# Optimization experiments

Hardware: AMD Instinct MI355X
Metric: run time of the kernel (lower is better)

The kernel has to match this reference:

```python
import jax, jax.numpy as jnp
import numpy as np

N_HEADS = 16
NEG_BIG = float(-2**32 + 1)  # value the original writes into masked positions


def setup_inputs() -> dict:
    key = jax.random.key(0)
    ks = jax.random.split(key, 5)
    B, T, D = 64, 256, 1024
    s = 1.0 / np.sqrt(D)
    return {
        "x": jax.random.normal(ks[0], (B, T, D), jnp.float32),
        "pos_emb": jax.random.normal(ks[1], (T, D), jnp.float32),
        "Wq": jax.random.normal(ks[2], (D, D), jnp.float32) * s,
        "Wk": jax.random.normal(ks[3], (D, D), jnp.float32) * s,
        "Wv": jax.random.normal(ks[4], (D, D), jnp.float32) * s,
    }


def reference(x, pos_emb, Wq, Wk, Wv):
    B, T, D = x.shape
    H = N_HEADS
    dh = D // H
    # add position embeddings (same arange positions for every batch row)
    temporal = x + pos_emb[None, :T, :]            # [B, T, D]
    q = temporal @ Wq                              # [B, T, D]
    k = temporal @ Wk
    v = temporal @ Wv
    # chunk along feature dim into H heads, concatenate along batch dim -> [H*B, T, dh]
    def split_heads(t):
        return jnp.concatenate(jnp.split(t, H, axis=2), axis=0)
    q_, k_, v_ = split_heads(q), split_heads(k), split_heads(v)
    scores = jnp.einsum('btd,bsd->bts', q_, k_) / jnp.sqrt(jnp.asarray(T, x.dtype))  # [H*B, T, T]
    # original masks the LOWER triangle (tril > 0 -> padding), faithful to source
    tril = jnp.tril(jnp.ones((T, T), x.dtype))
    scores = jnp.where(tril > 0, jnp.asarray(NEG_BIG, x.dtype), scores)
    # original applies softmax over dim=0 (the batch*head axis), faithful to source
    probs = jax.nn.softmax(scores, axis=0)         # [H*B, T, T]
    out = jnp.einsum('bts,bsd->btd', probs, v_)    # [H*B, T, dh]
    # merge heads back: chunk along batch dim, concatenate along feature dim
    out = jnp.concatenate(jnp.split(out, H, axis=0), axis=-1)  # [B, T, D]
    return out
```

## Files before the change

kernel.cpp:

```cpp
#include <hip/hip_runtime.h>

constexpr int SEQ = 256;
constexpr int DIM = 1024;
constexpr float SCALE = 0.0625f;

typedef __attribute__((ext_vector_type(8))) short bf16x8;
typedef __attribute__((ext_vector_type(4))) float f32x4;
typedef unsigned short ushort_t;
typedef unsigned int uint_t;

__device__ __forceinline__ void gld_lds16(const void* g, void* l) {
  __builtin_amdgcn_global_load_lds(
      (const __attribute__((address_space(1))) unsigned int*)g,
      (__attribute__((address_space(3))) unsigned int*)l, 16, 0, 0);
}

__device__ __forceinline__ ushort_t f2bf(float f) {
  uint_t u = __float_as_uint(f);
  return (ushort_t)((u + 0x7fffu + ((u >> 16) & 1u)) >> 16);
}

__global__ __launch_bounds__(256)
void prep_a(const float* __restrict__ x, const float* __restrict__ pos,
            ushort_t* __restrict__ Ab) {
  const size_t idx = ((size_t)blockIdx.x * 256 + threadIdx.x) * 8;
  const int m = (int)(idx >> 10), k = (int)(idx & 1023);
  float4 x0 = *(const float4*)(x + idx);
  float4 x1 = *(const float4*)(x + idx + 4);
  const float* pp = pos + ((size_t)(m & 255) << 10) + k;
  float4 p0 = *(const float4*)pp;
  float4 p1 = *(const float4*)(pp + 4);
  uint_t w0 = (uint_t)f2bf(x0.x + p0.x) | ((uint_t)f2bf(x0.y + p0.y) << 16);
  uint_t w1 = (uint_t)f2bf(x0.z + p0.z) | ((uint_t)f2bf(x0.w + p0.w) << 16);
  uint_t w2 = (uint_t)f2bf(x1.x + p1.x) | ((uint_t)f2bf(x1.y + p1.y) << 16);
  uint_t w3 = (uint_t)f2bf(x1.z + p1.z) | ((uint_t)f2bf(x1.w + p1.w) << 16);
  *(uint4*)&Ab[idx] = make_uint4(w0, w1, w2, w3);
}

__global__ __launch_bounds__(256)
void pack_w(const float* __restrict__ Wq, const float* __restrict__ Wk,
            const float* __restrict__ Wv, ushort_t* __restrict__ Bp) {
  const float* W = (blockIdx.z == 0) ? Wq : (blockIdx.z == 1) ? Wk : Wv;
  const int n  = blockIdx.x * 256 + threadIdx.x;
  const int k8 = blockIdx.y * 8;
  uint_t h[8];
#pragma unroll
  for (int i = 0; i < 8; ++i) h[i] = f2bf(W[(size_t)(k8 + i) * DIM + n]);
  uint_t hp[4];
#pragma unroll
  for (int j = 0; j < 4; ++j) hp[j] = h[2 * j] | (h[2 * j + 1] << 16);
  const int np = blockIdx.z * 1024 + n;
  const int nb = np >> 8, nl = np & 255;
  const int kc = k8 >> 6, kk = k8 & 63;
  size_t base = (((size_t)nb * 16 + kc) * 256 + nl) * 64 + kk;
  *(uint4*)&Bp[base] = make_uint4(hp[0], hp[1], hp[2], hp[3]);
}

__global__ __launch_bounds__(512, 2)
void qkv_mfma(const ushort_t* __restrict__ Ab, const ushort_t* __restrict__ Bp,
              ushort_t* __restrict__ q_bf, ushort_t* __restrict__ k_bf,
              ushort_t* __restrict__ vT_bf) {
  const int nb = blockIdx.x;
  const int mb = blockIdx.y;
  const int tid = (int)threadIdx.x;
  const int wave = tid >> 6, lane = tid & 63;
  const int wm = wave >> 2, wn = wave & 3;
  const int l15 = lane & 15, quad = lane >> 4;

  __shared__ ushort_t smem[65536];

  const int r8 = lane >> 3;
  const int lc8 = ((lane & 7) ^ r8) * 8;
  const size_t a_row = ((size_t)(mb * 256 + wave * 8 + r8)) << 10;
  const size_t b_row = ((size_t)((nb * 16) * 256 + wave * 8 + r8)) << 6;
  const int wb = wave * 512;

#define SA(q, tt, c) gld_lds16(Ab + a_row + ((size_t)(q) << 16) + (size_t)(tt) * 64 + lc8, \
                               smem + (c) * 32768 + (q) * 4096 + wb)
#define SB(q, tt, c) gld_lds16(Bp + b_row + (size_t)(tt) * 16384 + (q) * 4096 + lc8, \
                               smem + (c) * 32768 + 16384 + (q) * 4096 + wb)

  const int swz = l15 & 7;
  const int cko0 = (quad ^ swz) * 8;
  const int cko1 = ((4 + quad) ^ swz) * 8;
  const int arow0 = (wm * 128 + l15) * 64;
  const int brow0 = (wn * 64 + l15) * 64;

  f32x4 acc[8][4] = {};
  bf16x8 a_cur[4][2], b_all[4][2];

#define LDA(IH) do { _Pragma("unroll") for (int ii = 0; ii < 4; ++ii) { \
    const int ro = arow0 + ((IH) * 64 + ii * 16) * 64; \
    a_cur[ii][0] = *(const bf16x8*)&Ac[ro + cko0]; \
    a_cur[ii][1] = *(const bf16x8*)&Ac[ro + cko1]; } } while (0)
#define LDB(J) do { const int ro = brow0 + (J) * 1024; \
    b_all[J][0] = *(const bf16x8*)&Bc[ro + cko0]; \
    b_all[J][1] = *(const bf16x8*)&Bc[ro + cko1]; } while (0)
#define MM(IH, J0) do { \
    asm volatile("s_waitcnt lgkmcnt(0)" ::: "memory"); \
    __builtin_amdgcn_s_setprio(1); \
    _Pragma("unroll") for (int ks = 0; ks < 2; ++ks) \
    _Pragma("unroll") for (int ii = 0; ii < 4; ++ii) \
    _Pragma("unroll") for (int jj = 0; jj < 2; ++jj) \
      acc[(IH)*4+ii][(J0)+jj] = __builtin_amdgcn_mfma_f32_16x16x32_bf16( \
          a_cur[ii][ks], b_all[(J0)+jj][ks], acc[(IH)*4+ii][(J0)+jj], 0, 0, 0); \
    __builtin_amdgcn_s_setprio(0); } while (0)

  SA(0, 0, 0); SA(2, 0, 0); SB(0, 0, 0); SB(1, 0, 0); SB(2, 0, 0); SB(3, 0, 0);
  SA(1, 0, 0); SA(3, 0, 0);
  SB(0, 1, 1); SB(1, 1, 1); SA(0, 1, 1); SA(2, 1, 1);
  asm volatile("s_waitcnt vmcnt(6)" ::: "memory");
  __builtin_amdgcn_s_barrier();

  for (int t = 0; t < 16; ++t) {
    const int cur = t & 1, nxt = cur ^ 1;
    const int tn  = (t < 15) ? t + 1 : 15;
    const int tn2 = (t < 14) ? t + 2 : 15;
    const ushort_t* Ac = &smem[cur * 32768];
    const ushort_t* Bc = Ac + 16384;
    LDA(0); LDB(0); LDB(1);
    SB(2, tn, nxt); SB(3, tn, nxt);
    __builtin_amdgcn_s_barrier();
    MM(0, 0);
    __builtin_amdgcn_s_barrier();
    LDB(2); LDB(3);
    SA(1, tn, nxt); SA(3, tn, nxt);
    __builtin_amdgcn_s_barrier();
    MM(0, 2);
    asm volatile("s_waitcnt vmcnt(8)" ::: "memory");
    __builtin_amdgcn_s_barrier();
    LDA(1);
    SB(0, tn2, cur); SB(1, tn2, cur);
    __builtin_amdgcn_s_barrier();
    MM(1, 2);
    __builtin_amdgcn_s_barrier();
    SA(0, tn2, cur); SA(2, tn2, cur);
    __builtin_amdgcn_s_barrier();
    MM(1, 0);
    asm volatile("s_waitcnt vmcnt(6)" ::: "memory");
    __builtin_amdgcn_s_barrier();
  }

  asm volatile("s_waitcnt vmcnt(0)" ::: "memory");
  const int wq = nb >> 2;
  const int h  = (nb & 3) * 4 + wn;
  if (wq < 2) {
    ushort_t* base = ((wq == 0) ? q_bf : k_bf) + (size_t)(mb * 16 + h) * (SEQ * 64);
    const int tb = wm * 128 + quad * 4;
#pragma unroll
    for (int i = 0; i < 8; ++i)
#pragma unroll
      for (int j = 0; j < 4; ++j) {
        const int d = j * 16 + l15;
#pragma unroll
        for (int r = 0; r < 4; ++r)
          base[(size_t)(tb + i * 16 + r) * 64 + d] = f2bf(acc[i][j][r]);
      }
  } else {
    __builtin_amdgcn_s_barrier();
    ushort_t* L = &smem[wave * 4608];
    ushort_t* vbase = vT_bf + (size_t)(mb * 16 + h) * (64 * SEQ) + wm * 128;
    const int tc = (lane & 7) * 8;
#pragma unroll
    for (int g = 0; g < 2; ++g) {
#pragma unroll
      for (int ii = 0; ii < 4; ++ii)
#pragma unroll
        for (int j = 0; j < 4; ++j) {
          f32x4 v = acc[g * 4 + ii][j];
          uint_t lo = (uint_t)f2bf(v[0]) | ((uint_t)f2bf(v[1]) << 16);
          uint_t hi = (uint_t)f2bf(v[2]) | ((uint_t)f2bf(v[3]) << 16);
          *(uint2*)&L[(j * 16 + l15) * 72 + ii * 16 + quad * 4] = make_uint2(lo, hi);
        }
#pragma unroll
      for (int u = 0; u < 8; ++u) {
        const int d = u * 8 + r8;
        uint4 val = *(const uint4*)&L[d * 72 + tc];
        *(uint4*)&vbase[(size_t)d * SEQ + g * 64 + tc] = val;
      }
    }
  }
#undef SA
#undef SB
#undef LDA
#undef LDB
#undef MM
}

__global__ __launch_bounds__(256)
void stats_mfma(const ushort_t* __restrict__ qb, const ushort_t* __restrict__ kb,
                float* __restrict__ part_l) {
  const int p = blockIdx.x, g = blockIdx.y;
  int tt, ss;
  if (p < 4) { tt = p; ss = p; }
  else {
    const int idx = p - 4;
    tt = (idx < 3) ? 0 : (idx < 5) ? 1 : 2;
    ss = (idx < 3) ? idx + 1 : (idx < 5) ? idx - 1 : 3;
  }
  const bool diag = (p < 4);
  const int tid = threadIdx.x, wave = tid >> 6, lane = tid & 63;
  const int l15 = lane & 15, quad = lane >> 4;
  const int slot = g * 4 + wave;

  f32x4 lacc[4][4] = {};

  for (int i4 = 0; i4 < 4; ++i4) {
    const int bp = slot * 4 + i4;
    const int bh = (bp & 63) * 16 + (bp >> 6);
    const ushort_t* qt = qb + (size_t)bh * (SEQ * 64) + (size_t)(tt * 64) * 64;
    const ushort_t* kt = kb + (size_t)bh * (SEQ * 64) + (size_t)(ss * 64) * 64;
    bf16x8 aq[4][2], bk[4][2];
#pragma unroll
    for (int m = 0; m < 4; ++m)
#pragma unroll
      for (int ks = 0; ks < 2; ++ks) {
        aq[m][ks] = *(const bf16x8*)&qt[(m * 16 + l15) * 64 + ks * 32 + quad * 8];
        bk[m][ks] = *(const bf16x8*)&kt[(m * 16 + l15) * 64 + ks * 32 + quad * 8];
      }
    f32x4 sf[4][4] = {};
#pragma unroll
    for (int ks = 0; ks < 2; ++ks)
#pragma unroll
      for (int m = 0; m < 4; ++m)
#pragma unroll
        for (int n = 0; n < 4; ++n)
          sf[m][n] = __builtin_amdgcn_mfma_f32_16x16x32_bf16(aq[m][ks], bk[n][ks], sf[m][n], 0, 0, 0);
#pragma unroll
    for (int m = 0; m < 4; ++m)
#pragma unroll
      for (int n = 0; n < 4; ++n)
#pragma unroll
        for (int r = 0; r < 4; ++r) {
          float e = __expf(sf[m][n][r] * SCALE);
          if (diag) {
            const int t = tt * 64 + m * 16 + quad * 4 + r;
            const int s = ss * 64 + n * 16 + l15;
            e = (s > t) ? e : 1.0f;
          }
          lacc[m][n][r] += e;
        }
  }
  float* pl = part_l + (size_t)slot * (SEQ * SEQ);
#pragma unroll
  for (int m = 0; m < 4; ++m)
#pragma unroll
    for (int r = 0; r < 4; ++r) {
      const int t = tt * 64 + m * 16 + quad * 4 + r;
#pragma unroll
      for (int n = 0; n < 4; ++n)
        pl[(size_t)t * SEQ + ss * 64 + n * 16 + l15] = lacc[m][n][r];
    }
}

__global__ __launch_bounds__(256)
void merge_kernel(const float* __restrict__ part_l, float* __restrict__ inv_lT) {
  const int i = blockIdx.x * 256 + threadIdx.x;
  const int t = i >> 8, s = i & 255;
  float invv;
  if (s <= t) invv = 1.0f / 1024.0f;
  else {
    const float* p = part_l + i;
    float a0 = 0.f, a1 = 0.f, a2 = 0.f, a3 = 0.f,
          a4 = 0.f, a5 = 0.f, a6 = 0.f, a7 = 0.f;
    for (int g = 0; g < 256; g += 8) {
      const float* q = p + ((size_t)g << 16);
      a0 += q[0ull << 16]; a1 += q[1ull << 16]; a2 += q[2ull << 16]; a3 += q[3ull << 16];
      a4 += q[4ull << 16]; a5 += q[5ull << 16]; a6 += q[6ull << 16]; a7 += q[7ull << 16];
    }
    invv = 1.0f / (((a0 + a1) + (a2 + a3)) + ((a4 + a5) + (a6 + a7)));
  }
  inv_lT[s * SEQ + t] = invv;
}

__global__ __launch_bounds__(256)
void pv_mfma(const ushort_t* __restrict__ qb, const ushort_t* __restrict__ kb,
             const ushort_t* __restrict__ vtb, const float* __restrict__ inv_lT,
             float* __restrict__ out) {
  const int bh = blockIdx.x;
  const int b = bh >> 4, h = bh & 15;
  const int tid = threadIdx.x, wave = tid >> 6, lane = tid & 63;
  const int l15 = lane & 15, quad = lane >> 4;
  const int t0 = wave * 64;

  __shared__ ushort_t Plds[4][64][72];
  ushort_t (*Pw)[72] = Plds[wave];

  const ushort_t* qq = qb + (size_t)bh * (SEQ * 64);
  const ushort_t* kk = kb + (size_t)bh * (SEQ * 64);
  const ushort_t* vv = vtb + (size_t)bh * (64 * SEQ);

  bf16x8 qf[4][2];
#pragma unroll
  for (int nt = 0; nt < 4; ++nt)
#pragma unroll
    for (int ks = 0; ks < 2; ++ks)
      qf[nt][ks] = *(const bf16x8*)&qq[(t0 + nt * 16 + l15) * 64 + ks * 32 + quad * 8];

  f32x4 o[4][4] = {};

  for (int sc = 0; sc < 4; ++sc) {
    if (sc < wave) {
      const uint_t c = 0x3A803A80u;
      const uint4 cc = make_uint4(c, c, c, c);
#pragma unroll
      for (int u = 0; u < 8; ++u) *(uint4*)&Pw[lane][u * 8] = cc;
    } else {
      bf16x8 kf[4][2];
#pragma unroll
      for (int ms = 0; ms < 4; ++ms)
#pragma unroll
        for (int ks = 0; ks < 2; ++ks)
          kf[ms][ks] = *(const bf16x8*)&kk[(sc * 64 + ms * 16 + l15) * 64 + ks * 32 + quad * 8];
      f32x4 sf[4][4] = {};
#pragma unroll
      for (int ks = 0; ks < 2; ++ks)
#pragma unroll
        for (int ms = 0; ms < 4; ++ms)
#pragma unroll
          for (int nt = 0; nt < 4; ++nt)
            sf[ms][nt] = __builtin_amdgcn_mfma_f32_16x16x32_bf16(kf[ms][ks], qf[nt][ks], sf[ms][nt], 0, 0, 0);
      const bool dg = (sc == wave);
      const int t = t0 + l15;
#pragma unroll
      for (int ms = 0; ms < 4; ++ms)
#pragma unroll
        for (int nt = 0; nt < 4; ++nt) {
          const int sb = sc * 64 + ms * 16 + quad * 4;
          const int tc = t + nt * 16;
          ushort_t pb[4];
#pragma unroll
          for (int r = 0; r < 4; ++r) {
            const int s = sb + r;
            float e = __expf(sf[ms][nt][r] * SCALE);
            if (dg) e = (s > tc) ? e : 1.0f;
            pb[r] = f2bf(e * inv_lT[(size_t)s * SEQ + tc]);
          }
          uint_t lo = (uint_t)pb[0] | ((uint_t)pb[1] << 16);
          uint_t hi = (uint_t)pb[2] | ((uint_t)pb[3] << 16);
          *(uint2*)&Pw[nt * 16 + l15][ms * 16 + quad * 4] = make_uint2(lo, hi);
        }
    }
    bf16x8 vf[4][2], pf[4][2];
#pragma unroll
    for (int nd = 0; nd < 4; ++nd)
#pragma unroll
      for (int ks = 0; ks < 2; ++ks)
        vf[nd][ks] = *(const bf16x8*)&vv[(nd * 16 + l15) * SEQ + sc * 64 + ks * 32 + quad * 8];
#pragma unroll
    for (int mt = 0; mt < 4; ++mt)
#pragma unroll
      for (int ks = 0; ks < 2; ++ks)
        pf[mt][ks] = *(const bf16x8*)&Pw[mt * 16 + l15][ks * 32 + quad * 8];
#pragma unroll
    for (int ks = 0; ks < 2; ++ks)
#pragma unroll
      for (int mt = 0; mt < 4; ++mt)
#pragma unroll
        for (int nd = 0; nd < 4; ++nd)
          o[mt][nd] = __builtin_amdgcn_mfma_f32_16x16x32_bf16(pf[mt][ks], vf[nd][ks], o[mt][nd], 0, 0, 0);
  }

  float* ob = out + (size_t)b * SEQ * DIM + h * 64;
#pragma unroll
  for (int mt = 0; mt < 4; ++mt)
#pragma unroll
    for (int r = 0; r < 4; ++r) {
      const int t = t0 + mt * 16 + quad * 4 + r;
#pragma unroll
      for (int nd = 0; nd < 4; ++nd)
        ob[(size_t)t * DIM + nd * 16 + l15] = o[mt][nd][r];
    }
}

extern "C" void kernel_launch(void* const* d_in, const int* in_sizes, int n_in,
                              void* d_out, int out_size, void* d_ws, size_t ws_size,
                              hipStream_t stream) {
  const float* x   = (const float*)d_in[0];
  const float* pos = (const float*)d_in[1];
  const float* Wq  = (const float*)d_in[2];
  const float* Wk  = (const float*)d_in[3];
  const float* Wv  = (const float*)d_in[4];
  float* out = (float*)d_out;

  ushort_t* Ab = (ushort_t*)d_out;
  ushort_t* Bp = (ushort_t*)((char*)d_out + 33554432);

  char* W = (char*)d_ws;
  ushort_t* q_bf   = (ushort_t*)(W);
  ushort_t* k_bf   = (ushort_t*)(W + 33554432);
  ushort_t* vT_bf  = (ushort_t*)(W + 67108864);
  float*    part_l = (float*)  (W + 100663296);
  float*    inv_lT = (float*)  (W + 167772160);

  prep_a<<<dim3(8192), 256, 0, stream>>>(x, pos, Ab);
  pack_w<<<dim3(4, 128, 3), 256, 0, stream>>>(Wq, Wk, Wv, Bp);
  qkv_mfma<<<dim3(12, 64), 512, 0, stream>>>(Ab, Bp, q_bf, k_bf, vT_bf);
  stats_mfma<<<dim3(10, 64), 256, 0, stream>>>(q_bf, k_bf, part_l);
  merge_kernel<<<dim3(SEQ * SEQ / 256), 256, 0, stream>>>(part_l, inv_lT);
  pv_mfma<<<dim3(1024), 256, 0, stream>>>(q_bf, k_bf, vT_bf, inv_lT, out);
}
```

Baseline: 366.1 us.

## Reschedule GEMM LDS loads with MFMAs and reduce stats partials in shared memory

The projection GEMM main loop drops several barriers and splits the MFMA blocks into quarters. Fragment LDS reads are interleaved with MFMA issue under partial lgkmcnt waits, so LDS latency is hidden inside compute. The stats kernel now sums the four waves' partial exp-sums in shared memory before writing, which cuts the partial buffer from 256 slots to 64. The merge kernel then reads a quarter of the data. The risk is that the looser barrier and waitcnt schedule could race on double-buffered LDS, and the larger shared-memory footprint may lower occupancy in the stats kernel.

```diff
diff --git a/kernel.cpp b/kernel.cpp
--- a/kernel.cpp
+++ b/kernel.cpp
@@ -87,24 +87,22 @@
   const int brow0 = (wn * 64 + l15) * 64;
 
   f32x4 acc[8][4] = {};
-  bf16x8 a_cur[4][2], b_all[4][2];
-
-#define LDA(IH) do { _Pragma("unroll") for (int ii = 0; ii < 4; ++ii) { \
-    const int ro = arow0 + ((IH) * 64 + ii * 16) * 64; \
-    a_cur[ii][0] = *(const bf16x8*)&Ac[ro + cko0]; \
-    a_cur[ii][1] = *(const bf16x8*)&Ac[ro + cko1]; } } while (0)
-#define LDB(J) do { const int ro = brow0 + (J) * 1024; \
-    b_all[J][0] = *(const bf16x8*)&Bc[ro + cko0]; \
-    b_all[J][1] = *(const bf16x8*)&Bc[ro + cko1]; } while (0)
-#define MM(IH, J0) do { \
-    asm volatile("s_waitcnt lgkmcnt(0)" ::: "memory"); \
-    __builtin_amdgcn_s_setprio(1); \
+  bf16x8 af[4][2], bf[4][2];
+
+#define LDA_II(IH, ii) do { \
+    const int ro = arow0 + ((IH) * 64 + (ii) * 16) * 64; \
+    af[ii][0] = *(const bf16x8*)&Ac[ro + cko0]; \
+    af[ii][1] = *(const bf16x8*)&Ac[ro + cko1]; } while (0)
+#define LDB_J(J) do { const int ro = brow0 + (J) * 1024; \
+    bf[J][0] = *(const bf16x8*)&Bc[ro + cko0]; \
+    bf[J][1] = *(const bf16x8*)&Bc[ro + cko1]; } while (0)
+#define MMQ(IH, II0, II1, J0) do { \
     _Pragma("unroll") for (int ks = 0; ks < 2; ++ks) \
-    _Pragma("unroll") for (int ii = 0; ii < 4; ++ii) \
+    _Pragma("unroll") for (int ii = (II0); ii < (II1); ++ii) \
     _Pragma("unroll") for (int jj = 0; jj < 2; ++jj) \
-      acc[(IH)*4+ii][(J0)+jj] = __builtin_amdgcn_mfma_f32_16x16x32_bf16( \
-          a_cur[ii][ks], b_all[(J0)+jj][ks], acc[(IH)*4+ii][(J0)+jj], 0, 0, 0); \
-    __builtin_amdgcn_s_setprio(0); } while (0)
+      acc[(IH) * 4 + ii][(J0) + jj] = __builtin_amdgcn_mfma_f32_16x16x32_bf16( \
+          af[ii][ks], bf[(J0) + jj][ks], acc[(IH) * 4 + ii][(J0) + jj], 0, 0, 0); \
+    } while (0)
 
   SA(0, 0, 0); SA(2, 0, 0); SB(0, 0, 0); SB(1, 0, 0); SB(2, 0, 0); SB(3, 0, 0);
   SA(1, 0, 0); SA(3, 0, 0);
@@ -118,25 +116,38 @@
     const int tn2 = (t < 14) ? t + 2 : 15;
     const ushort_t* Ac = &smem[cur * 32768];
     const ushort_t* Bc = Ac + 16384;
-    LDA(0); LDB(0); LDB(1);
+    LDA_II(0, 0); LDA_II(0, 1); LDA_II(0, 2); LDA_II(0, 3);
+    LDB_J(0); LDB_J(1);
     SB(2, tn, nxt); SB(3, tn, nxt);
     __builtin_amdgcn_s_barrier();
-    MM(0, 0);
-    __builtin_amdgcn_s_barrier();
-    LDB(2); LDB(3);
+    LDB_J(2); LDB_J(3);
     SA(1, tn, nxt); SA(3, tn, nxt);
-    __builtin_amdgcn_s_barrier();
-    MM(0, 2);
+    asm volatile("s_waitcnt lgkmcnt(4)" ::: "memory");
+    __builtin_amdgcn_s_setprio(1);
+    MMQ(0, 0, 4, 0);
+    __builtin_amdgcn_s_setprio(0);
     asm volatile("s_waitcnt vmcnt(8)" ::: "memory");
     __builtin_amdgcn_s_barrier();
-    LDA(1);
+    asm volatile("s_waitcnt lgkmcnt(0)" ::: "memory");
+    __builtin_amdgcn_s_setprio(1);
+    MMQ(0, 0, 2, 2);
+    __builtin_amdgcn_s_setprio(0);
+    LDA_II(1, 0); LDA_II(1, 1);
+    __builtin_amdgcn_s_setprio(1);
+    MMQ(0, 2, 4, 2);
+    __builtin_amdgcn_s_setprio(0);
+    LDA_II(1, 2); LDA_II(1, 3);
+    __builtin_amdgcn_s_barrier();
     SB(0, tn2, cur); SB(1, tn2, cur);
-    __builtin_amdgcn_s_barrier();
-    MM(1, 2);
+    asm volatile("s_waitcnt lgkmcnt(0)" ::: "memory");
+    __builtin_amdgcn_s_setprio(1);
+    MMQ(1, 0, 4, 2);
+    __builtin_amdgcn_s_setprio(0);
     __builtin_amdgcn_s_barrier();
     SA(0, tn2, cur); SA(2, tn2, cur);
-    __builtin_amdgcn_s_barrier();
-    MM(1, 0);
+    __builtin_amdgcn_s_setprio(1);
+    MMQ(1, 0, 4, 0);
+    __builtin_amdgcn_s_setprio(0);
     asm volatile("s_waitcnt vmcnt(6)" ::: "memory");
     __builtin_amdgcn_s_barrier();
   }
@@ -182,9 +193,9 @@
   }
 #undef SA
 #undef SB
-#undef LDA
-#undef LDB
-#undef MM
+#undef LDA_II
+#undef LDB_J
+#undef MMQ
 }
 
 __global__ __launch_bounds__(256)
@@ -201,12 +212,13 @@
   const bool diag = (p < 4);
   const int tid = threadIdx.x, wave = tid >> 6, lane = tid & 63;
   const int l15 = lane & 15, quad = lane >> 4;
-  const int slot = g * 4 + wave;
+
+  __shared__ __attribute__((aligned(16))) float red[4][64 * 68];
 
   f32x4 lacc[4][4] = {};
 
   for (int i4 = 0; i4 < 4; ++i4) {
-    const int bp = slot * 4 + i4;
+    const int bp = g * 16 + wave * 4 + i4;
     const int bh = (bp & 63) * 16 + (bp >> 6);
     const ushort_t* qt = qb + (size_t)bh * (SEQ * 64) + (size_t)(tt * 64) * 64;
     const ushort_t* kt = kb + (size_t)bh * (SEQ * 64) + (size_t)(ss * 64) * 64;
@@ -241,16 +253,36 @@
           lacc[m][n][r] += e;
         }
   }
-  float* pl = part_l + (size_t)slot * (SEQ * SEQ);
+  float* R = red[wave];
 #pragma unroll
   for (int m = 0; m < 4; ++m)
 #pragma unroll
     for (int r = 0; r < 4; ++r) {
-      const int t = tt * 64 + m * 16 + quad * 4 + r;
+      const int row = m * 16 + quad * 4 + r;
 #pragma unroll
       for (int n = 0; n < 4; ++n)
-        pl[(size_t)t * SEQ + ss * 64 + n * 16 + l15] = lacc[m][n][r];
+        R[row * 68 + n * 16 + l15] = lacc[m][n][r];
     }
+  __syncthreads();
+  const int trow = tid >> 2, c0 = (tid & 3) * 16;
+  const float* r0 = &red[0][trow * 68 + c0];
+  const float* r1 = &red[1][trow * 68 + c0];
+  const float* r2 = &red[2][trow * 68 + c0];
+  const float* r3 = &red[3][trow * 68 + c0];
+  float* pl = part_l + (size_t)g * (SEQ * SEQ) + (size_t)(tt * 64 + trow) * SEQ + ss * 64 + c0;
+#pragma unroll
+  for (int c = 0; c < 16; c += 4) {
+    float4 s0 = *(const float4*)&r0[c];
+    float4 s1 = *(const float4*)&r1[c];
+    float4 s2 = *(const float4*)&r2[c];
+    float4 s3 = *(const float4*)&r3[c];
+    float4 o;
+    o.x = (s0.x + s1.x) + (s2.x + s3.x);
+    o.y = (s0.y + s1.y) + (s2.y + s3.y);
+    o.z = (s0.z + s1.z) + (s2.z + s3.z);
+    o.w = (s0.w + s1.w) + (s2.w + s3.w);
+    *(float4*)&pl[c] = o;
+  }
 }
 
 __global__ __launch_bounds__(256)
@@ -263,7 +295,7 @@
     const float* p = part_l + i;
     float a0 = 0.f, a1 = 0.f, a2 = 0.f, a3 = 0.f,
           a4 = 0.f, a5 = 0.f, a6 = 0.f, a7 = 0.f;
-    for (int g = 0; g < 256; g += 8) {
+    for (int g = 0; g < 64; g += 8) {
       const float* q = p + ((size_t)g << 16);
       a0 += q[0ull << 16]; a1 += q[1ull << 16]; a2 += q[2ull << 16]; a3 += q[3ull << 16];
       a4 += q[4ull << 16]; a5 += q[5ull << 16]; a6 += q[6ull << 16]; a7 += q[7ull << 16];
```

After: 350.7 us. 1.04x faster.
